# Kernel tuning notes

Measured on AMD Instinct MI355X. Metric: run time of the kernel, lower is better.

## Reference

```python
import jax, jax.numpy as jnp
import numpy as np

D_MODEL = 1024
HEADS = 16
D_KEY = D_MODEL // HEADS


def setup_inputs() -> dict:
    key = jax.random.key(0)
    ks = jax.random.split(key, 7)
    B, S = 4, 2048
    queries = jax.random.normal(ks[0], (B, S, D_MODEL), dtype=jnp.float32)
    keys = jax.random.normal(ks[1], (B, S, D_MODEL), dtype=jnp.float32)
    values = jax.random.normal(ks[2], (B, S, D_MODEL), dtype=jnp.float32)
    scale = 1.0 / np.sqrt(D_MODEL)
    # Per-head projection weights, torch Linear layout [out=d_key, in=d_model], stacked over heads
    Wq = jax.random.uniform(ks[3], (HEADS, D_KEY, D_MODEL), jnp.float32, -scale, scale)
    Wk = jax.random.uniform(ks[4], (HEADS, D_KEY, D_MODEL), jnp.float32, -scale, scale)
    Wv = jax.random.uniform(ks[5], (HEADS, D_KEY, D_MODEL), jnp.float32, -scale, scale)
    Wo = jax.random.uniform(ks[6], (D_MODEL, D_MODEL), jnp.float32, -scale, scale)
    return {"queries": queries, "keys": keys, "values": values,
            "Wq": Wq, "Wk": Wk, "Wv": Wv, "Wo": Wo}


def reference(queries, keys, values, Wq, Wk, Wv, Wo):
    # Project per head: [B,S,D] x [H,K,D] -> [B,H,S,K]
    q = jnp.einsum('bsd,hkd->bhsk', queries, Wq)
    k = jnp.einsum('bsd,hkd->bhsk', keys, Wk)
    v = jnp.einsum('bsd,hkd->bhsk', values, Wv)
    attn = jnp.einsum('bhqk,bhsk->bhqs', q, k) / jnp.sqrt(jnp.float32(D_KEY))
    attn = jax.nn.softmax(attn, axis=-1)
    out = jnp.einsum('bhqs,bhsk->bhqk', attn, v)  # [B,H,S,K]
    B, H, S, K = out.shape
    # concat heads along last dim (head order = torch cat order)
    out = out.transpose(0, 2, 1, 3).reshape(B, S, H * K)
    return out @ Wo.T
```

## Files before the change

### kernel.cpp

```cpp
#include <hip/hip_runtime.h>
#include <hip/hip_bf16.h>

typedef __attribute__((ext_vector_type(8))) short short8;
typedef __attribute__((ext_vector_type(4))) short short4v;
typedef __attribute__((ext_vector_type(4))) float f32x4;
typedef __bf16 bf16x8 __attribute__((ext_vector_type(8)));

#define DEVI static __device__ __forceinline__

DEVI short f2bs(float f) {
    union { __hip_bfloat16 h; short s; } u;
    u.h = __float2bfloat16(f);
    return u.s;
}

DEVI f32x4 mfma16(short8 a, short8 b, f32x4 c) {
    return __builtin_amdgcn_mfma_f32_16x16x32_bf16(
        __builtin_bit_cast(bf16x8, a), __builtin_bit_cast(bf16x8, b), c, 0, 0, 0);
}

DEVI void glds16(const short* g, short* l) {
    __builtin_amdgcn_global_load_lds((const __attribute__((address_space(1))) void*)g,
                                     (__attribute__((address_space(3))) void*)l, 16, 0, 0);
}

__global__ __launch_bounds__(256) void cvt_all(const float4* __restrict__ q,
                                               const float4* __restrict__ k,
                                               const float4* __restrict__ v,
                                               const float4* __restrict__ wq,
                                               const float4* __restrict__ wk,
                                               const float4* __restrict__ wv,
                                               const float4* __restrict__ wo,
                                               short4v* __restrict__ dq,
                                               short4v* __restrict__ dk,
                                               short4v* __restrict__ dv,
                                               short4v* __restrict__ dwq,
                                               short4v* __restrict__ dwk,
                                               short4v* __restrict__ dwv,
                                               short4v* __restrict__ dwo) {
    int bid = blockIdx.x;
    float4 x;
    short4v s;
    if (bid < 8192) {
        int i = bid * 256 + threadIdx.x;
        x = q[i]; s.x = f2bs(x.x); s.y = f2bs(x.y); s.z = f2bs(x.z); s.w = f2bs(x.w); dq[i] = s;
        x = k[i]; s.x = f2bs(x.x); s.y = f2bs(x.y); s.z = f2bs(x.z); s.w = f2bs(x.w); dk[i] = s;
        x = v[i]; s.x = f2bs(x.x); s.y = f2bs(x.y); s.z = f2bs(x.z); s.w = f2bs(x.w); dv[i] = s;
    } else {
        int i = (bid - 8192) * 256 + threadIdx.x;
        x = wq[i]; s.x = f2bs(x.x); s.y = f2bs(x.y); s.z = f2bs(x.z); s.w = f2bs(x.w); dwq[i] = s;
        x = wk[i]; s.x = f2bs(x.x); s.y = f2bs(x.y); s.z = f2bs(x.z); s.w = f2bs(x.w); dwk[i] = s;
        x = wv[i]; s.x = f2bs(x.x); s.y = f2bs(x.y); s.z = f2bs(x.z); s.w = f2bs(x.w); dwv[i] = s;
        x = wo[i]; s.x = f2bs(x.x); s.y = f2bs(x.y); s.z = f2bs(x.z); s.w = f2bs(x.w); dwo[i] = s;
    }
}

template <typename EpiT>
DEVI void gemm_body(const short* A, const short* Bw, short* smem, int m0, int n0, EpiT epi) {
    short* As = smem;
    short* Bs = smem + 8192;
    const int t = threadIdx.x;
    const int lane = t & 63, w = t >> 6;
    const int col = lane & 15, quad = lane >> 4;
    const int wm = (w & 1) * 64, wn = (w >> 1) * 64;

    f32x4 acc[4][4];
#pragma unroll
    for (int i = 0; i < 4; ++i)
#pragma unroll
        for (int j = 0; j < 4; ++j) acc[i][j] = (f32x4){0.f, 0.f, 0.f, 0.f};

    for (int kt = 0; kt < 16; ++kt) {
        const int k0 = kt * 64;
#pragma unroll
        for (int j = 0; j < 4; ++j) {
            int cbase = (j * 4 + w) * 64;
            int c = cbase + lane;
            int row = c >> 3, kc = (c & 7) ^ (row & 7);
            glds16(A + (size_t)(m0 + row) * 1024 + k0 + kc * 8, As + cbase * 8);
        }
#pragma unroll
        for (int j = 0; j < 4; ++j) {
            int cbase = (j * 4 + w) * 64;
            int c = cbase + lane;
            int row = c >> 3, kc = (c & 7) ^ (row & 7);
            glds16(Bw + (size_t)(n0 + row) * 1024 + k0 + kc * 8, Bs + cbase * 8);
        }
        __syncthreads();
#pragma unroll
        for (int ks = 0; ks < 2; ++ks) {
            short8 a[4], b[4];
#pragma unroll
            for (int i = 0; i < 4; ++i) {
                int row = wm + i * 16 + col;
                int kc = (ks * 4 + quad) ^ (col & 7);
                a[i] = *(const short8*)(As + (row * 8 + kc) * 8);
            }
#pragma unroll
            for (int i = 0; i < 4; ++i) {
                int row = wn + i * 16 + col;
                int kc = (ks * 4 + quad) ^ (col & 7);
                b[i] = *(const short8*)(Bs + (row * 8 + kc) * 8);
            }
#pragma unroll
            for (int mi = 0; mi < 4; ++mi)
#pragma unroll
                for (int ni = 0; ni < 4; ++ni)
                    acc[mi][ni] = mfma16(a[mi], b[ni], acc[mi][ni]);
        }
        __syncthreads();
    }
    epi(acc, wm, wn, col, quad);
}

__global__ __launch_bounds__(256) void qkv_gemm(const short* __restrict__ xq,
                                                const short* __restrict__ xk,
                                                const short* __restrict__ xv,
                                                const short* __restrict__ wq,
                                                const short* __restrict__ wk,
                                                const short* __restrict__ wv,
                                                short* __restrict__ qp,
                                                short* __restrict__ kp,
                                                short* __restrict__ vpt, float qscale) {
    __shared__ __align__(16) short smem[17408];
    const int z = blockIdx.z;
    const int m0 = blockIdx.y * 128, n0 = blockIdx.x * 128;
    const short* A = (z == 0) ? xq : (z == 1) ? xk : xv;
    const short* W = (z == 0) ? wq : (z == 1) ? wk : wv;

    if (z < 2) {
        short* outs = (z == 0) ? qp : kp;
        const float scale = (z == 0) ? qscale : 1.0f;
        gemm_body(A, W, smem, m0, n0, [&](f32x4 (&acc)[4][4], int wm, int wn, int col, int quad) {
            short* T = smem;
#pragma unroll
            for (int mi = 0; mi < 4; ++mi)
#pragma unroll
                for (int ni = 0; ni < 4; ++ni)
#pragma unroll
                    for (int r = 0; r < 4; ++r)
                        T[(wm + mi * 16 + quad * 4 + r) * 136 + wn + ni * 16 + col] =
                            f2bs(acc[mi][ni][r] * scale);
            __syncthreads();
            int t = threadIdx.x;
            int ml = t >> 1, nh = (t & 1) * 64;
            int m = m0 + ml;
            int b = m >> 11, s = m & 2047;
#pragma unroll
            for (int j = 0; j < 8; ++j) {
                int n = n0 + nh + j * 8;
                short8 vv = *(const short8*)(T + ml * 136 + nh + j * 8);
                size_t off = ((size_t)(b * 16 + (n >> 6)) * 2048 + s) * 64 + (n & 63);
                *(short8*)(outs + off) = vv;
            }
        });
    } else {
        gemm_body(A, W, smem, m0, n0, [&](f32x4 (&acc)[4][4], int wm, int wn, int col, int quad) {
            short* T = smem;
#pragma unroll
            for (int mi = 0; mi < 4; ++mi)
#pragma unroll
                for (int ni = 0; ni < 4; ++ni) {
                    int n_l = wn + ni * 16 + col;
                    int m_l = wm + mi * 16 + quad * 4;
                    short4v sv;
                    sv.x = f2bs(acc[mi][ni][0]); sv.y = f2bs(acc[mi][ni][1]);
                    sv.z = f2bs(acc[mi][ni][2]); sv.w = f2bs(acc[mi][ni][3]);
                    *(short4v*)(T + n_l * 132 + m_l) = sv;
                }
            __syncthreads();
            int t = threadIdx.x;
            int nrow = t >> 1, mh = (t & 1) * 64;
            int b = m0 >> 11, s0 = m0 & 2047;
            size_t base = ((size_t)(b * 1024 + n0 + nrow)) * 2048 + s0 + mh;
#pragma unroll
            for (int j = 0; j < 16; ++j) {
                unsigned long long vv = *(const unsigned long long*)(T + nrow * 132 + mh + j * 4);
                *(unsigned long long*)(vpt + base + j * 4) = vv;
            }
        });
    }
}

__global__ __launch_bounds__(256) void out_gemm(const short* __restrict__ ao,
                                                const short* __restrict__ wo,
                                                float* __restrict__ outf) {
    __shared__ __align__(16) short smem[16896];
    const int m0 = blockIdx.y * 128, n0 = blockIdx.x * 128;
    gemm_body(ao, wo, smem, m0, n0, [&](f32x4 (&acc)[4][4], int wm, int wn, int col, int quad) {
#pragma unroll
        for (int mi = 0; mi < 4; ++mi)
#pragma unroll
            for (int ni = 0; ni < 4; ++ni)
#pragma unroll
                for (int r = 0; r < 4; ++r) {
                    int m = m0 + wm + mi * 16 + quad * 4 + r;
                    int n = n0 + wn + ni * 16 + col;
                    outf[(size_t)m * 1024 + n] = acc[mi][ni][r];
                }
    });
}

__global__ __launch_bounds__(256, 4) void flash_attn(const short* __restrict__ qp,
                                                     const short* __restrict__ kp,
                                                     const short* __restrict__ vpt,
                                                     short* __restrict__ ao) {
    __shared__ __align__(16) short smem[8192 + 8192 + 4096];
    short* Ks = smem;
    short* Vs = smem + 8192;

    const int t = threadIdx.x, lane = t & 63, w = t >> 6;
    const int col = lane & 15, quad = lane >> 4;
    const int bh = blockIdx.x, q0 = blockIdx.y * 128;
    const short* qb = qp + (size_t)bh * 2048 * 64;
    const short* kb = kp + (size_t)bh * 2048 * 64;
    const short* vb = vpt + (size_t)bh * 64 * 2048;
    short* Pw = smem + 16384 + w * 1024;

#pragma unroll
    for (int j = 0; j < 4; ++j) {
        int cbase = (j * 4 + w) * 64;
        int c = cbase + lane;
        int row = c >> 3, kc = (c & 7) ^ (row & 7);
        glds16(qb + (size_t)(q0 + row) * 64 + kc * 8, Ks + cbase * 8);
    }
    __syncthreads();
    short8 bQ[2][2];
#pragma unroll
    for (int qi = 0; qi < 2; ++qi)
#pragma unroll
        for (int ks = 0; ks < 2; ++ks) {
            int row = w * 32 + qi * 16 + col;
            int kc = (ks * 4 + quad) ^ (col & 7);
            bQ[qi][ks] = *(const short8*)(Ks + (row * 8 + kc) * 8);
        }
    __syncthreads();

    f32x4 acc_o[2][4];
    float l_r[2] = {0.f, 0.f};
#pragma unroll
    for (int qi = 0; qi < 2; ++qi)
#pragma unroll
        for (int ni = 0; ni < 4; ++ni) acc_o[qi][ni] = (f32x4){0.f, 0.f, 0.f, 0.f};

    for (int kt = 0; kt < 16; ++kt) {
#pragma unroll
        for (int j = 0; j < 4; ++j) {
            int cbase = (j * 4 + w) * 64;
            int c = cbase + lane;
            int row = c >> 3, kc = (c & 7) ^ (row & 7);
            glds16(kb + (size_t)(kt * 128 + row) * 64 + kc * 8, Ks + cbase * 8);
        }
#pragma unroll
        for (int j = 0; j < 4; ++j) {
            int m = w * 4 + j;
            int dk = m * 4 + (lane >> 4);
            int sc = (lane & 15) ^ (dk & 15);
            glds16(vb + (size_t)dk * 2048 + kt * 128 + sc * 8, Vs + m * 512);
        }
        __syncthreads();

#pragma unroll
        for (int g = 0; g < 4; ++g) {
#pragma unroll
            for (int h = 0; h < 2; ++h) {
                int kei = g * 2 + h;
                f32x4 st[2];
                st[0] = (f32x4){0.f, 0.f, 0.f, 0.f};
                st[1] = (f32x4){0.f, 0.f, 0.f, 0.f};
#pragma unroll
                for (int ks = 0; ks < 2; ++ks) {
                    int row = kei * 16 + col;
                    int kc = (ks * 4 + quad) ^ (col & 7);
                    short8 aK = *(const short8*)(Ks + (row * 8 + kc) * 8);
#pragma unroll
                    for (int qi = 0; qi < 2; ++qi) st[qi] = mfma16(aK, bQ[qi][ks], st[qi]);
                }
#pragma unroll
                for (int qi = 0; qi < 2; ++qi) {
                    float p0 = __builtin_amdgcn_exp2f(st[qi][0]);
                    float p1 = __builtin_amdgcn_exp2f(st[qi][1]);
                    float p2 = __builtin_amdgcn_exp2f(st[qi][2]);
                    float p3 = __builtin_amdgcn_exp2f(st[qi][3]);
                    l_r[qi] += (p0 + p1) + (p2 + p3);
                    short4v pv;
                    pv.x = f2bs(p0); pv.y = f2bs(p1); pv.z = f2bs(p2); pv.w = f2bs(p3);
                    int row = qi * 16 + col;
                    int ch = (h * 2 + (quad >> 1)) ^ (row & 3);
                    *(short4v*)(Pw + row * 32 + ch * 8 + (quad & 1) * 4) = pv;
                }
            }
            short8 pa[2];
#pragma unroll
            for (int qi = 0; qi < 2; ++qi) {
                int row = qi * 16 + col;
                pa[qi] = *(const short8*)(Pw + row * 32 + (quad ^ (row & 3)) * 8);
            }
#pragma unroll
            for (int ni = 0; ni < 4; ++ni) {
                int dk = ni * 16 + col;
                short8 bv = *(const short8*)(Vs + dk * 128 + (((g * 4 + quad) ^ col) * 8));
#pragma unroll
                for (int qi = 0; qi < 2; ++qi)
                    acc_o[qi][ni] = mfma16(pa[qi], bv, acc_o[qi][ni]);
            }
        }
        __syncthreads();
    }

#pragma unroll
    for (int qi = 0; qi < 2; ++qi) {
        l_r[qi] += __shfl_xor(l_r[qi], 16);
        l_r[qi] += __shfl_xor(l_r[qi], 32);
    }
    const int b = bh >> 4, hd = bh & 15;
#pragma unroll
    for (int qi = 0; qi < 2; ++qi)
#pragma unroll
        for (int r = 0; r < 4; ++r) {
            float lq = __shfl(l_r[qi], quad * 4 + r);
            float inv = 1.0f / lq;
            int q = q0 + w * 32 + qi * 16 + quad * 4 + r;
#pragma unroll
            for (int ni = 0; ni < 4; ++ni)
                ao[((size_t)(b * 2048 + q)) * 1024 + hd * 64 + ni * 16 + col] =
                    f2bs(acc_o[qi][ni][r] * inv);
        }
}

extern "C" void kernel_launch(void* const* d_in, const int* in_sizes, int n_in,
                              void* d_out, int out_size, void* d_ws, size_t ws_size,
                              hipStream_t stream) {
    const float* q  = (const float*)d_in[0];
    const float* k  = (const float*)d_in[1];
    const float* v  = (const float*)d_in[2];
    const float* Wq = (const float*)d_in[3];
    const float* Wk = (const float*)d_in[4];
    const float* Wv = (const float*)d_in[5];
    const float* Wo = (const float*)d_in[6];
    float* out = (float*)d_out;

    short* ws = (short*)d_ws;
    const size_t SZ = (size_t)64 * 2048 * 64;
    const size_t WZ = (size_t)1024 * 1024;
    short* xq  = ws;
    short* xk  = ws + SZ;
    short* xv  = ws + 2 * SZ;
    short* qp  = ws + 3 * SZ;
    short* kp  = ws + 4 * SZ;
    short* wqb = ws + 5 * SZ;
    short* wkb = wqb + WZ;
    short* wvb = wqb + 2 * WZ;
    short* wob = wqb + 3 * WZ;
    short* ao  = xq;
    short* vpt = xk;

    const float QSCALE = 0.125f * 1.44269504088896f;

    cvt_all<<<dim3(9216), dim3(256), 0, stream>>>(
        (const float4*)q, (const float4*)k, (const float4*)v, (const float4*)Wq,
        (const float4*)Wk, (const float4*)Wv, (const float4*)Wo, (short4v*)xq, (short4v*)xk,
        (short4v*)xv, (short4v*)wqb, (short4v*)wkb, (short4v*)wvb, (short4v*)wob);
    dim3 blk(256);
    qkv_gemm<<<dim3(8, 64, 3), blk, 0, stream>>>(xq, xk, xv, wqb, wkb, wvb, qp, kp, vpt, QSCALE);
    flash_attn<<<dim3(64, 16), blk, 0, stream>>>(qp, kp, vpt, ao);
    out_gemm<<<dim3(8, 64), blk, 0, stream>>>(ao, wob, out);
}
```

Baseline: 353.0 us.

## Redistribute softmax P via permlane swaps instead of LDS round-trip; add setprio

The P tile (exp of scores, packed to bf16) is no longer written to and read back from per-wave LDS. It is rearranged into the MFMA A-operand layout entirely in registers using v_permlane32_swap and v_permlane16_swap, which frees 8 KB of shared memory per block. s_setprio is also raised around the MFMA sections so waves in their matrix phase get issue priority over others. This removes LDS traffic and latency from the inner loop and lowers LDS use, at the cost of relying on the permlane swaps producing exactly the right lane mapping.

```diff
diff --git a/kernel.cpp b/kernel.cpp
--- a/kernel.cpp
+++ b/kernel.cpp
@@ -5,6 +5,8 @@
 typedef __attribute__((ext_vector_type(4))) short short4v;
 typedef __attribute__((ext_vector_type(4))) float f32x4;
 typedef __bf16 bf16x8 __attribute__((ext_vector_type(8)));
+typedef __attribute__((ext_vector_type(2))) unsigned int u32x2;
+typedef __attribute__((ext_vector_type(4))) unsigned int u32x4;
 
 #define DEVI static __device__ __forceinline__
 
@@ -12,6 +14,25 @@
     union { __hip_bfloat16 h; short s; } u;
     u.h = __float2bfloat16(f);
     return u.s;
+}
+
+DEVI unsigned pack2(float a, float b) {
+    union { short s[2]; unsigned u; } u;
+    u.s[0] = f2bs(a);
+    u.s[1] = f2bs(b);
+    return u.u;
+}
+
+DEVI void xchg(unsigned& x, unsigned& y) {
+#if __has_builtin(__builtin_amdgcn_permlane32_swap) && __has_builtin(__builtin_amdgcn_permlane16_swap)
+    u32x2 t = __builtin_amdgcn_permlane32_swap(x, y, false, false);
+    u32x2 r = __builtin_amdgcn_permlane16_swap(t[0], t[1], false, false);
+    x = r[0];
+    y = r[1];
+#else
+    asm("v_permlane32_swap_b32 %0, %1" : "+v"(x), "+v"(y));
+    asm("v_permlane16_swap_b32 %0, %1" : "+v"(x), "+v"(y));
+#endif
 }
 
 DEVI f32x4 mfma16(short8 a, short8 b, f32x4 c) {
@@ -205,7 +226,7 @@
                                                      const short* __restrict__ kp,
                                                      const short* __restrict__ vpt,
                                                      short* __restrict__ ao) {
-    __shared__ __align__(16) short smem[8192 + 8192 + 4096];
+    __shared__ __align__(16) short smem[8192 + 8192];
     short* Ks = smem;
     short* Vs = smem + 8192;
 
@@ -215,7 +236,6 @@
     const short* qb = qp + (size_t)bh * 2048 * 64;
     const short* kb = kp + (size_t)bh * 2048 * 64;
     const short* vb = vpt + (size_t)bh * 64 * 2048;
-    short* Pw = smem + 16384 + w * 1024;
 
 #pragma unroll
     for (int j = 0; j < 4; ++j) {
@@ -262,12 +282,14 @@
 
 #pragma unroll
         for (int g = 0; g < 4; ++g) {
+            unsigned pdw[2][4];
 #pragma unroll
             for (int h = 0; h < 2; ++h) {
                 int kei = g * 2 + h;
                 f32x4 st[2];
                 st[0] = (f32x4){0.f, 0.f, 0.f, 0.f};
                 st[1] = (f32x4){0.f, 0.f, 0.f, 0.f};
+                __builtin_amdgcn_s_setprio(1);
 #pragma unroll
                 for (int ks = 0; ks < 2; ++ks) {
                     int row = kei * 16 + col;
@@ -276,6 +298,7 @@
 #pragma unroll
                     for (int qi = 0; qi < 2; ++qi) st[qi] = mfma16(aK, bQ[qi][ks], st[qi]);
                 }
+                __builtin_amdgcn_s_setprio(0);
 #pragma unroll
                 for (int qi = 0; qi < 2; ++qi) {
                     float p0 = __builtin_amdgcn_exp2f(st[qi][0]);
@@ -283,19 +306,19 @@
                     float p2 = __builtin_amdgcn_exp2f(st[qi][2]);
                     float p3 = __builtin_amdgcn_exp2f(st[qi][3]);
                     l_r[qi] += (p0 + p1) + (p2 + p3);
-                    short4v pv;
-                    pv.x = f2bs(p0); pv.y = f2bs(p1); pv.z = f2bs(p2); pv.w = f2bs(p3);
-                    int row = qi * 16 + col;
-                    int ch = (h * 2 + (quad >> 1)) ^ (row & 3);
-                    *(short4v*)(Pw + row * 32 + ch * 8 + (quad & 1) * 4) = pv;
+                    pdw[qi][h * 2]     = pack2(p0, p1);
+                    pdw[qi][h * 2 + 1] = pack2(p2, p3);
                 }
             }
             short8 pa[2];
 #pragma unroll
             for (int qi = 0; qi < 2; ++qi) {
-                int row = qi * 16 + col;
-                pa[qi] = *(const short8*)(Pw + row * 32 + (quad ^ (row & 3)) * 8);
-            }
+                xchg(pdw[qi][0], pdw[qi][2]);
+                xchg(pdw[qi][1], pdw[qi][3]);
+                u32x4 pv = {pdw[qi][0], pdw[qi][1], pdw[qi][2], pdw[qi][3]};
+                pa[qi] = __builtin_bit_cast(short8, pv);
+            }
+            __builtin_amdgcn_s_setprio(1);
 #pragma unroll
             for (int ni = 0; ni < 4; ++ni) {
                 int dk = ni * 16 + col;
@@ -304,6 +327,7 @@
                 for (int qi = 0; qi < 2; ++qi)
                     acc_o[qi][ni] = mfma16(pa[qi], bv, acc_o[qi][ni]);
             }
+            __builtin_amdgcn_s_setprio(0);
         }
         __syncthreads();
     }
```

Result: faster. 344.0 us (-2.6%).
